# Performance work log

Hardware: AMD Instinct MI355X
Metric: run time of the kernel (lower is better)

The kernel has to match this reference:

```python
import jax, jax.numpy as jnp
import numpy as np

MX, SX = 0.0, 1.0  # msx
MY, SY = 0.0, 1.0  # msy


def _mode_linear(inp, phase, w, b):
    # Equivalent to: w_p = einsum('ji,imk->jmk', phase, w); out = squeeze(inp[:,None,:] @ w_p) + phase @ b
    # Fused blended form avoids the (batch, in, out) per-sample weight intermediate.
    out = jnp.einsum('bd,idh,bi->bh', inp, w, phase)
    return out + phase @ b


def setup_inputs() -> dict:
    key = jax.random.key(0)
    ks = jax.random.split(key, 4)
    B, D_IN, H, D_OUT = 32768, 256, 1024, 64
    x = jax.random.normal(ks[0], (B, D_IN + 2), dtype=jnp.float32)
    w1 = jax.random.normal(ks[1], (2, D_IN, H), dtype=jnp.float32) * 0.05
    b1 = jnp.zeros((2, H), dtype=jnp.float32)
    w2 = jax.random.normal(ks[2], (2, H, H), dtype=jnp.float32) * 0.05
    b2 = jnp.zeros((2, H), dtype=jnp.float32)
    w3 = jax.random.normal(ks[3], (2, H, D_OUT), dtype=jnp.float32) * 0.05
    b3 = jnp.zeros((2, D_OUT), dtype=jnp.float32)
    return {"x": x, "w1": w1, "b1": b1, "w2": w2, "b2": b2, "w3": w3, "b3": b3}


def reference(x, w1, b1, w2, b2, w3, b3):
    phase = x[:, -2:]                 # unscaled phase weights, per original code
    xs = (x - MX) / SX
    h = xs[:, :-2]                    # [B, D_IN]
    out = jax.nn.elu(_mode_linear(h, phase, w1, b1))
    out = jax.nn.elu(_mode_linear(out, phase, w2, b2))
    out = _mode_linear(out, phase, w3, b3)
    return out * SY + MY
```

## Files before the change

kernel.cpp:

```cpp
#include <hip/hip_runtime.h>

typedef unsigned short u16;
typedef __bf16 bf16x8 __attribute__((ext_vector_type(8)));
typedef float f32x4 __attribute__((ext_vector_type(4)));

#define AS1 __attribute__((address_space(1)))
#define AS3 __attribute__((address_space(3)))

static __device__ __forceinline__ u16 f2bf(float f) {
  union { float f; unsigned u; } v; v.f = f;
  unsigned r = (v.u + 0x7fff + ((v.u >> 16) & 1)) >> 16;
  return (u16)r;
}

__global__ void prep_x_kernel(const float* __restrict__ x, u16* __restrict__ hx,
                              float2* __restrict__ phase, int B) {
  int i = blockIdx.x * blockDim.x + threadIdx.x;
  int total = B * 128;
  if (i < total) {
    int row = i >> 7, k2 = (i & 127);
    const float2 v = *reinterpret_cast<const float2*>(x + (size_t)row * 258 + k2 * 2);
    u16 a = f2bf(v.x), b = f2bf(v.y);
    *reinterpret_cast<unsigned*>(hx + (size_t)row * 256 + k2 * 2) =
        (unsigned)a | ((unsigned)b << 16);
  }
  if (i < B) {
    phase[i] = *reinterpret_cast<const float2*>(x + (size_t)i * 258 + 256);
  }
}

__global__ void prep_w_kernel(const float* __restrict__ w, u16* __restrict__ wt,
                              int K, int N) {
  __shared__ u16 tile[64][65];
  int k0 = blockIdx.x * 64, n0 = blockIdx.y * 64, mode = blockIdx.z;
  const float* src = w + (size_t)mode * K * N;
  u16* dst = wt + (size_t)mode * N * K;
  int c = threadIdx.x & 63;
  int r4 = threadIdx.x >> 6;
#pragma unroll
  for (int i = 0; i < 16; ++i) {
    int r = r4 + i * 4;
    tile[r][c] = f2bf(src[(size_t)(k0 + r) * N + n0 + c]);
  }
  __syncthreads();
#pragma unroll
  for (int i = 0; i < 16; ++i) {
    int r = r4 + i * 4;
    dst[(size_t)(n0 + r) * K + k0 + c] = tile[c][r];
  }
}

__global__ void prep_w_int_kernel(const float* __restrict__ w, u16* __restrict__ wt,
                                  int K, int N) {
  __shared__ u16 tile[64][65];
  int k0 = blockIdx.x * 64, n0 = blockIdx.y * 64, mode = blockIdx.z;
  const float* src = w + (size_t)mode * K * N;
  int c = threadIdx.x & 63;
  int r4 = threadIdx.x >> 6;
#pragma unroll
  for (int i = 0; i < 16; ++i) {
    int r = r4 + i * 4;
    tile[r][c] = f2bf(src[(size_t)(k0 + r) * N + n0 + c]);
  }
  __syncthreads();
#pragma unroll
  for (int i = 0; i < 16; ++i) {
    int n = n0 + r4 + i * 4;
    int np = ((n >> 4) << 5) + (mode << 4) + (n & 15);
    wt[(size_t)np * K + k0 + c] = tile[c][r4 + i * 4];
  }
}

template <bool ELU_STORE>
__global__ __launch_bounds__(512, 2) void gemm_ring(
    const u16* __restrict__ A, const u16* __restrict__ Wt,
    const float* __restrict__ bias, const float2* __restrict__ phase,
    u16* __restrict__ out, int K, int Np) {
  __shared__ u16 lds[4][2][8192];
  const int tnc = Np >> 8;
  const int nwg = gridDim.x;
  int id = blockIdx.x;
  const int cpx = nwg >> 3;
  id = (id & 7) * cpx + (id >> 3);
  const int m0 = (id / tnc) * 256;
  const int n0 = (id % tnc) * 256;
  const int t = threadIdx.x;
  const int lane = t & 63;
  const int wave = t >> 6;
  const int wr = wave >> 2, wc = wave & 3;
  const int lr = lane & 15, ks = lane >> 4;
  const int cswz = lr * 64 + (((ks * 8) ^ ((lr >> 3) << 4)) << 1);

  int soff[2];
#pragma unroll
  for (int ld = 0; ld < 2; ++ld) {
    int e = (ld * 512 + t) * 8;
    int st = e >> 9;
    int rl = (e >> 5) & 15;
    int c = e & 31;
    int c0 = c ^ (((rl >> 3) & 1) << 4);
    soff[ld] = (st * 16 + rl) * K + c0;
  }
  const u16* Abase = A + (size_t)m0 * K;
  const u16* Bbase = Wt + (size_t)n0 * K;

  f32x4 acc[8][4] = {};
  const int NT = K >> 5;

  auto stage = [&](int bb, int tile) {
    const int kt = tile << 5;
#pragma unroll
    for (int ld = 0; ld < 2; ++ld)
      __builtin_amdgcn_global_load_lds(
          (const AS1 void*)(Abase + kt + soff[ld]),
          (AS3 void*)(&lds[bb][0][(ld * 512 + t) * 8]), 16, 0, 0);
#pragma unroll
    for (int ld = 0; ld < 2; ++ld)
      __builtin_amdgcn_global_load_lds(
          (const AS1 void*)(Bbase + kt + soff[ld]),
          (AS3 void*)(&lds[bb][1][(ld * 512 + t) * 8]), 16, 0, 0);
  };

#define BAR()                    \
  asm volatile("" ::: "memory"); \
  __builtin_amdgcn_s_barrier();  \
  asm volatile("" ::: "memory");

#define LOADA0(buf)                               \
  _Pragma("unroll") for (int m = 0; m < 4; ++m)   \
      af0[m] = *(const bf16x8*)((const char*)&lds[buf][0][0] + (((wr * 8 + m) << 10) + cswz));
#define LOADA1(buf)                               \
  _Pragma("unroll") for (int m = 0; m < 4; ++m)   \
      af1[m] = *(const bf16x8*)((const char*)&lds[buf][0][0] + (((wr * 8 + 4 + m) << 10) + cswz));
#define LOADB(buf)                                \
  _Pragma("unroll") for (int n = 0; n < 4; ++n)   \
      bfr[n] = *(const bf16x8*)((const char*)&lds[buf][1][0] + (((wc * 4 + n) << 10) + cswz));
#define MFMAH(mh, AF)                                                   \
  __builtin_amdgcn_s_setprio(1);                                        \
  _Pragma("unroll") for (int m = 0; m < 4; ++m)                         \
  _Pragma("unroll") for (int n = 0; n < 4; ++n)                         \
      acc[(mh)*4 + m][n] = __builtin_amdgcn_mfma_f32_16x16x32_bf16(     \
          AF[m], bfr[n], acc[(mh)*4 + m][n], 0, 0, 0);                  \
  __builtin_amdgcn_s_setprio(0);

  bf16x8 af0[4], af1[4], bfr[4];

  stage(0, 0);
  stage(1, 1);
  stage(2, 2);
  asm volatile("s_waitcnt vmcnt(8)" ::: "memory");
  BAR();
  LOADA0(0);
  LOADB(0);

  for (int tt = 0; tt < NT; ++tt) {
    const int b = tt & 3;
    LOADA1(b);
    MFMAH(0, af0);
    if (tt + 3 < NT) stage((tt + 3) & 3, tt + 3);
    asm volatile("s_waitcnt vmcnt(8)" ::: "memory");
    MFMAH(1, af1);
    BAR();
    if (tt + 1 < NT) {
      const int b2 = (tt + 1) & 3;
      LOADA0(b2);
      LOADB(b2);
    }
  }
#undef LOADA0
#undef LOADA1
#undef LOADB
#undef MFMAH

  const int Nreal = Np >> 1;
  const int colbase = (n0 + wc * 64) >> 1;
  float bias0[2], bias1[2];
#pragma unroll
  for (int pj = 0; pj < 2; ++pj) {
    int ncol = colbase + pj * 16 + lr;
    bias0[pj] = bias[ncol];
    bias1[pj] = bias[Nreal + ncol];
  }
#pragma unroll
  for (int m = 0; m < 8; ++m) {
#pragma unroll
    for (int j = 0; j < 4; ++j) {
      int grow = m0 + wr * 128 + m * 16 + ks * 4 + j;
      float2 ph = phase[grow];
#pragma unroll
      for (int pj = 0; pj < 2; ++pj) {
        int ncol = colbase + pj * 16 + lr;
        float v = ph.x * (acc[m][pj * 2 + 0][j] + bias0[pj]) +
                  ph.y * (acc[m][pj * 2 + 1][j] + bias1[pj]);
        if (ELU_STORE) v = v > 0.f ? v : (__expf(v) - 1.f);
        out[(size_t)grow * Nreal + ncol] = f2bf(v);
      }
    }
  }
#undef BAR
}

template <int BM, int BN, int WM, int WN, bool ELU_BF16>
__launch_bounds__(256, 2) __global__
void gemm_dualmode(const u16* __restrict__ A, const u16* __restrict__ WT,
                   const float* __restrict__ bias, const float2* __restrict__ phase,
                   void* __restrict__ out, int K, int N) {
  constexpr int MF = WM / 16, NF = WN / 16;
  __shared__ u16 ldsA[BM * 32];
  __shared__ u16 ldsB[2][BN * 32];
  const int m0 = blockIdx.x * BM;
  const int n0 = blockIdx.y * BN;
  const int t = threadIdx.x;
  const int wave = t >> 6, lane = t & 63;
  constexpr int NWC = BN / WN;
  const int wr = wave / NWC, wc = wave % NWC;
  const int lr = lane & 15, ks = lane >> 4;

  f32x4 acc[2][MF][NF] = {};

  for (int kt = 0; kt < K; kt += 32) {
#pragma unroll
    for (int i = 0; i < BM / 64; ++i) {
      int tt = t + i * 256;
      int r = tt >> 2, c8 = (tt & 3) * 8;
      __builtin_amdgcn_global_load_lds(
          (const AS1 void*)(A + (size_t)(m0 + r) * K + kt + c8),
          (AS3 void*)(ldsA + (size_t)tt * 8), 16, 0, 0);
    }
#pragma unroll
    for (int md = 0; md < 2; ++md) {
#pragma unroll
      for (int i = 0; i < BN / 64; ++i) {
        int tt = t + i * 256;
        int r = tt >> 2, c8 = (tt & 3) * 8;
        __builtin_amdgcn_global_load_lds(
            (const AS1 void*)(WT + (size_t)md * N * K + (size_t)(n0 + r) * K + kt + c8),
            (AS3 void*)(ldsB[md] + (size_t)tt * 8), 16, 0, 0);
      }
    }
    __syncthreads();

    bf16x8 af[MF], b0f[NF], b1f[NF];
#pragma unroll
    for (int m = 0; m < MF; ++m)
      af[m] = *reinterpret_cast<const bf16x8*>(&ldsA[(wr * WM + m * 16 + lr) * 32 + ks * 8]);
#pragma unroll
    for (int n = 0; n < NF; ++n) {
      b0f[n] = *reinterpret_cast<const bf16x8*>(&ldsB[0][(wc * WN + n * 16 + lr) * 32 + ks * 8]);
      b1f[n] = *reinterpret_cast<const bf16x8*>(&ldsB[1][(wc * WN + n * 16 + lr) * 32 + ks * 8]);
    }
#pragma unroll
    for (int m = 0; m < MF; ++m) {
#pragma unroll
      for (int n = 0; n < NF; ++n) {
        acc[0][m][n] = __builtin_amdgcn_mfma_f32_16x16x32_bf16(af[m], b0f[n], acc[0][m][n], 0, 0, 0);
        acc[1][m][n] = __builtin_amdgcn_mfma_f32_16x16x32_bf16(af[m], b1f[n], acc[1][m][n], 0, 0, 0);
      }
    }
    __syncthreads();
  }

#pragma unroll
  for (int m = 0; m < MF; ++m) {
#pragma unroll
    for (int j = 0; j < 4; ++j) {
      int grow = m0 + wr * WM + m * 16 + ks * 4 + j;
      float2 ph = phase[grow];
#pragma unroll
      for (int n = 0; n < NF; ++n) {
        int gcol = n0 + wc * WN + n * 16 + lr;
        float v = ph.x * (acc[0][m][n][j] + bias[gcol]) +
                  ph.y * (acc[1][m][n][j] + bias[N + gcol]);
        if (ELU_BF16) {
          v = v > 0.f ? v : (__expf(v) - 1.f);
          ((u16*)out)[(size_t)grow * N + gcol] = f2bf(v);
        } else {
          ((float*)out)[(size_t)grow * N + gcol] = v;
        }
      }
    }
  }
}

extern "C" void kernel_launch(void* const* d_in, const int* in_sizes, int n_in,
                              void* d_out, int out_size, void* d_ws, size_t ws_size,
                              hipStream_t stream) {
  const float* x  = (const float*)d_in[0];
  const float* w1 = (const float*)d_in[1];
  const float* b1 = (const float*)d_in[2];
  const float* w2 = (const float*)d_in[3];
  const float* b2 = (const float*)d_in[4];
  const float* w3 = (const float*)d_in[5];
  const float* b3 = (const float*)d_in[6];
  float* out = (float*)d_out;
  const int B = 32768, DIN = 256, H = 1024, DOUT = 64;

  char* ws = (char*)d_ws;
  u16* W1Ti = (u16*)ws;    ws += (size_t)2 * H * DIN * 2;
  u16* W2Ti = (u16*)ws;    ws += (size_t)2 * H * H * 2;
  u16* W3T = (u16*)ws;     ws += (size_t)2 * DOUT * H * 2;
  float2* phase = (float2*)ws; ws += (size_t)B * 8;
  u16* hx = (u16*)ws;      ws += (size_t)B * DIN * 2;
  u16* h1 = (u16*)ws;      ws += (size_t)B * H * 2;
  u16* h2 = (u16*)ws;      ws += (size_t)B * H * 2;

  prep_x_kernel<<<(B * 128 + 255) / 256, 256, 0, stream>>>(x, hx, phase, B);
  prep_w_int_kernel<<<dim3(DIN / 64, H / 64, 2), 256, 0, stream>>>(w1, W1Ti, DIN, H);
  prep_w_int_kernel<<<dim3(H / 64, H / 64, 2), 256, 0, stream>>>(w2, W2Ti, H, H);
  prep_w_kernel<<<dim3(H / 64, DOUT / 64, 2), 256, 0, stream>>>(w3, W3T, H, DOUT);

  const int nwg = (B / 256) * (2 * H / 256);
  gemm_ring<true><<<nwg, 512, 0, stream>>>(hx, W1Ti, b1, phase, h1, DIN, 2 * H);
  gemm_ring<true><<<nwg, 512, 0, stream>>>(h1, W2Ti, b2, phase, h2, H, 2 * H);
  gemm_dualmode<128, 64, 64, 32, false>
      <<<dim3(B / 128, DOUT / 64), 256, 0, stream>>>(h2, W3T, b3, phase, out, H, DOUT);
}
```

Measured before the change: 229.8 us.

## Shrink GEMM tile to 256x128 with 4 waves and triple-buffered LDS ring

The main bf16 GEMM moves from a 256x256 tile with 8 waves and a 4-deep LDS ring to a 256x128 tile with 4 waves and a 3-deep ring, with prefetch distance cut from 3 tiles to 2. The grid doubles, and LDS per block drops from 128KB to 72KB, so more blocks can be resident and there are more workgroups to fill the CUs. In exchange each block reuses its A tile over half as many columns, which adds global/L2 traffic for A, and the shallower prefetch gives less room to hide memory latency. The epilogue is left unchanged and is assumed to index correctly through wc with 2 column waves.

```diff
diff --git a/kernel.cpp b/kernel.cpp
--- a/kernel.cpp
+++ b/kernel.cpp
@@ -72,34 +72,37 @@
 }
 
 template <bool ELU_STORE>
-__global__ __launch_bounds__(512, 2) void gemm_ring(
+__global__ __launch_bounds__(256, 2) void gemm_ring3(
     const u16* __restrict__ A, const u16* __restrict__ Wt,
     const float* __restrict__ bias, const float2* __restrict__ phase,
     u16* __restrict__ out, int K, int Np) {
-  __shared__ u16 lds[4][2][8192];
-  const int tnc = Np >> 8;
+  __shared__ u16 lds[3][12288];
+  const int tnc = Np >> 7;
   const int nwg = gridDim.x;
   int id = blockIdx.x;
   const int cpx = nwg >> 3;
   id = (id & 7) * cpx + (id >> 3);
   const int m0 = (id / tnc) * 256;
-  const int n0 = (id % tnc) * 256;
+  const int n0 = (id % tnc) * 128;
   const int t = threadIdx.x;
   const int lane = t & 63;
   const int wave = t >> 6;
-  const int wr = wave >> 2, wc = wave & 3;
+  const int wr = wave >> 1, wc = wave & 1;
   const int lr = lane & 15, ks = lane >> 4;
   const int cswz = lr * 64 + (((ks * 8) ^ ((lr >> 3) << 4)) << 1);
 
-  int soff[2];
+  int soffA[4], soffB[2];
+#pragma unroll
+  for (int ld = 0; ld < 4; ++ld) {
+    int e = (ld * 256 + t) * 8;
+    int st = e >> 9, rl = (e >> 5) & 15, c = e & 31;
+    soffA[ld] = (st * 16 + rl) * K + (c ^ (((rl >> 3) & 1) << 4));
+  }
 #pragma unroll
   for (int ld = 0; ld < 2; ++ld) {
-    int e = (ld * 512 + t) * 8;
-    int st = e >> 9;
-    int rl = (e >> 5) & 15;
-    int c = e & 31;
-    int c0 = c ^ (((rl >> 3) & 1) << 4);
-    soff[ld] = (st * 16 + rl) * K + c0;
+    int e = (ld * 256 + t) * 8;
+    int st = e >> 9, rl = (e >> 5) & 15, c = e & 31;
+    soffB[ld] = (st * 16 + rl) * K + (c ^ (((rl >> 3) & 1) << 4));
   }
   const u16* Abase = A + (size_t)m0 * K;
   const u16* Bbase = Wt + (size_t)n0 * K;
@@ -110,15 +113,15 @@
   auto stage = [&](int bb, int tile) {
     const int kt = tile << 5;
 #pragma unroll
+    for (int ld = 0; ld < 4; ++ld)
+      __builtin_amdgcn_global_load_lds(
+          (const AS1 void*)(Abase + kt + soffA[ld]),
+          (AS3 void*)(&lds[bb][(ld * 256 + t) * 8]), 16, 0, 0);
+#pragma unroll
     for (int ld = 0; ld < 2; ++ld)
       __builtin_amdgcn_global_load_lds(
-          (const AS1 void*)(Abase + kt + soff[ld]),
-          (AS3 void*)(&lds[bb][0][(ld * 512 + t) * 8]), 16, 0, 0);
-#pragma unroll
-    for (int ld = 0; ld < 2; ++ld)
-      __builtin_amdgcn_global_load_lds(
-          (const AS1 void*)(Bbase + kt + soff[ld]),
-          (AS3 void*)(&lds[bb][1][(ld * 512 + t) * 8]), 16, 0, 0);
+          (const AS1 void*)(Bbase + kt + soffB[ld]),
+          (AS3 void*)(&lds[bb][8192 + (ld * 256 + t) * 8]), 16, 0, 0);
   };
 
 #define BAR()                    \
@@ -128,13 +131,13 @@
 
 #define LOADA0(buf)                               \
   _Pragma("unroll") for (int m = 0; m < 4; ++m)   \
-      af0[m] = *(const bf16x8*)((const char*)&lds[buf][0][0] + (((wr * 8 + m) << 10) + cswz));
+      af0[m] = *(const bf16x8*)((const char*)&lds[buf][0] + (((wr * 8 + m) << 10) + cswz));
 #define LOADA1(buf)                               \
   _Pragma("unroll") for (int m = 0; m < 4; ++m)   \
-      af1[m] = *(const bf16x8*)((const char*)&lds[buf][0][0] + (((wr * 8 + 4 + m) << 10) + cswz));
+      af1[m] = *(const bf16x8*)((const char*)&lds[buf][0] + (((wr * 8 + 4 + m) << 10) + cswz));
 #define LOADB(buf)                                \
   _Pragma("unroll") for (int n = 0; n < 4; ++n)   \
-      bfr[n] = *(const bf16x8*)((const char*)&lds[buf][1][0] + (((wc * 4 + n) << 10) + cswz));
+      bfr[n] = *(const bf16x8*)((const char*)&lds[buf][0] + 16384 + (((wc * 4 + n) << 10) + cswz));
 #define MFMAH(mh, AF)                                                   \
   __builtin_amdgcn_s_setprio(1);                                        \
   _Pragma("unroll") for (int m = 0; m < 4; ++m)                         \
@@ -147,25 +150,31 @@
 
   stage(0, 0);
   stage(1, 1);
-  stage(2, 2);
-  asm volatile("s_waitcnt vmcnt(8)" ::: "memory");
+  asm volatile("s_waitcnt vmcnt(6)" ::: "memory");
   BAR();
   LOADA0(0);
   LOADB(0);
 
+  int b = 0, b2 = 1, bs = 2;
   for (int tt = 0; tt < NT; ++tt) {
-    const int b = tt & 3;
     LOADA1(b);
     MFMAH(0, af0);
-    if (tt + 3 < NT) stage((tt + 3) & 3, tt + 3);
-    asm volatile("s_waitcnt vmcnt(8)" ::: "memory");
+    if (tt + 2 < NT) {
+      stage(bs, tt + 2);
+      asm volatile("s_waitcnt vmcnt(6)" ::: "memory");
+    } else {
+      asm volatile("s_waitcnt vmcnt(0)" ::: "memory");
+    }
     MFMAH(1, af1);
     BAR();
     if (tt + 1 < NT) {
-      const int b2 = (tt + 1) & 3;
       LOADA0(b2);
       LOADB(b2);
     }
+    int bn = b2;
+    b2 = bs;
+    bs = b;
+    b = bn;
   }
 #undef LOADA0
 #undef LOADA1
@@ -309,9 +318,9 @@
   prep_w_int_kernel<<<dim3(H / 64, H / 64, 2), 256, 0, stream>>>(w2, W2Ti, H, H);
   prep_w_kernel<<<dim3(H / 64, DOUT / 64, 2), 256, 0, stream>>>(w3, W3T, H, DOUT);
 
-  const int nwg = (B / 256) * (2 * H / 256);
-  gemm_ring<true><<<nwg, 512, 0, stream>>>(hx, W1Ti, b1, phase, h1, DIN, 2 * H);
-  gemm_ring<true><<<nwg, 512, 0, stream>>>(h1, W2Ti, b2, phase, h2, H, 2 * H);
+  const int nwg = (B / 256) * (2 * H / 128);
+  gemm_ring3<true><<<nwg, 256, 0, stream>>>(hx, W1Ti, b1, phase, h1, DIN, 2 * H);
+  gemm_ring3<true><<<nwg, 256, 0, stream>>>(h1, W2Ti, b2, phase, h2, H, 2 * H);
   gemm_dualmode<128, 64, 64, 32, false>
       <<<dim3(B / 128, DOUT / 64), 256, 0, stream>>>(h2, W3T, b3, phase, out, H, DOUT);
 }
```

After: 240.3 us. +4.6%, slower.
